# Performance work log

Measured on AMD Instinct MI355X. Metric: run time of the kernel, lower is better.

The kernel has to match this reference:

```python
import jax, jax.numpy as jnp
import numpy as np

HEADS = 32
KV_HEADS = 8
HEAD_DIM = 64
D = 2048
D_FF = 8192
EPS = 1e-6
THETA = 10000.0
MAX_STEPS = 4
NEG = -1e9


def _rope_tables(t):
    # LlamaRotaryEmbedding: cos/sin of shape [t, head_dim] with freqs duplicated
    inv_freq = 1.0 / (THETA ** (jnp.arange(0, HEAD_DIM, 2, dtype=jnp.float32) / HEAD_DIM))
    pos = jnp.arange(t, dtype=jnp.float32)
    freqs = pos[:, None] * inv_freq[None, :]          # [t, hd/2]
    emb = jnp.concatenate([freqs, freqs], axis=-1)    # [t, hd]
    return jnp.cos(emb), jnp.sin(emb)


def _rotate_half(x):
    h = x.shape[-1] // 2
    return jnp.concatenate([-x[..., h:], x[..., :h]], axis=-1)


def _rms_norm(x, w):
    return x * jax.lax.rsqrt(jnp.mean(x * x, axis=-1, keepdims=True) + EPS) * w


def _decoder_layer(h, w_q, w_k, w_v, w_o, ln1_w, ln2_w, w_gate, w_up, w_down):
    # h: [N, t, D]
    N, t, _ = h.shape
    x = _rms_norm(h, ln1_w)
    q = (x @ w_q).reshape(N, t, HEADS, HEAD_DIM)
    k = (x @ w_k).reshape(N, t, KV_HEADS, HEAD_DIM)
    v = (x @ w_v).reshape(N, t, KV_HEADS, HEAD_DIM)
    cos, sin = _rope_tables(t)
    cos = cos[None, :, None, :]
    sin = sin[None, :, None, :]
    q = q * cos + _rotate_half(q) * sin
    k = k * cos + _rotate_half(k) * sin
    rep = HEADS // KV_HEADS
    k = jnp.repeat(k, rep, axis=2)  # GQA: repeat kv heads
    v = jnp.repeat(v, rep, axis=2)
    scores = jnp.einsum('bqhd,bkhd->bhqk', q, k) / jnp.sqrt(jnp.float32(HEAD_DIM))
    causal = jnp.tril(jnp.ones((t, t), dtype=bool))
    scores = jnp.where(causal[None, None], scores, NEG)
    attn = jax.nn.softmax(scores, axis=-1)
    o = jnp.einsum('bhqk,bkhd->bqhd', attn, v).reshape(N, t, HEADS * HEAD_DIM)
    h = h + o @ w_o
    x = _rms_norm(h, ln2_w)
    h = h + (jax.nn.silu(x @ w_gate) * (x @ w_up)) @ w_down
    return h


def _micro_step_decode(hiddens, w_q, w_k, w_v, w_o, ln1_w, ln2_w, w_gate, w_up, w_down):
    # hiddens: [N, 1, D]; loop recomputes full attention over growing sequence (no KV cache)
    out = None
    for _ in range(MAX_STEPS + 1):
        out = _decoder_layer(hiddens, w_q, w_k, w_v, w_o, ln1_w, ln2_w, w_gate, w_up, w_down)
        hiddens = jnp.concatenate([hiddens, out[:, -1:, :]], axis=1)
    return out  # [N, MAX_STEPS+1, D]


def _gather_indices(comp_seq_lens, inst_lens):
    seqs = np.asarray(comp_seq_lens)
    insts = np.asarray(inst_lens)
    idx, off = [], 0
    for s, i in zip(seqs, insts):
        s, i = int(s), int(i)
        idx.append(np.arange(off + i - 1, off + s - 1))  # take_off_last=True
        off += s
    return np.concatenate(idx)


def setup_inputs() -> dict:
    key = jax.random.key(0)
    ks = jax.random.split(key, 10)
    B, S, I = 8, 512, 256
    total = B * S
    w = 0.02
    return {
        'hidden_states': jax.random.normal(ks[0], (1, total, D), jnp.float32),
        'comp_seq_lens': jnp.full((B,), S, dtype=jnp.int64),
        'inst_lens': jnp.full((B,), I, dtype=jnp.int64),
        'w_q': jax.random.normal(ks[1], (D, HEADS * HEAD_DIM), jnp.float32) * w,
        'w_k': jax.random.normal(ks[2], (D, KV_HEADS * HEAD_DIM), jnp.float32) * w,
        'w_v': jax.random.normal(ks[3], (D, KV_HEADS * HEAD_DIM), jnp.float32) * w,
        'w_o': jax.random.normal(ks[4], (HEADS * HEAD_DIM, D), jnp.float32) * w,
        'ln1_w': jnp.ones((D,), jnp.float32),
        'ln2_w': jnp.ones((D,), jnp.float32),
        'w_gate': jax.random.normal(ks[5], (D, D_FF), jnp.float32) * w,
        'w_up': jax.random.normal(ks[6], (D, D_FF), jnp.float32) * w,
        'w_down': jax.random.normal(ks[7], (D_FF, D), jnp.float32) * w,
    }


def reference(hidden_states, comp_seq_lens, inst_lens, w_q, w_k, w_v, w_o, ln1_w, ln2_w, w_gate, w_up, w_down):
    idx = _gather_indices(comp_seq_lens, inst_lens)
    hiddens = hidden_states[0, idx][:, None, :]  # [N, 1, D]
    return _micro_step_decode(hiddens, w_q, w_k, w_v, w_o, ln1_w, ln2_w, w_gate, w_up, w_down)
```

## Files before the change

### kernel.cpp

```cpp
#include <hip/hip_runtime.h>
#include <hip/hip_bf16.h>
#include <stdint.h>

#define DMODEL 2048
#define QDIM   2048
#define KVDIM  512
#define QKVDIM 3072
#define DFF    8192
#define NSTEPS 5

typedef __bf16 bf16_t;
typedef __attribute__((ext_vector_type(8))) __bf16 bf16x8;
typedef __attribute__((ext_vector_type(4))) float f32x4;

#define GLL16(g, l)                                                         \
  __builtin_amdgcn_global_load_lds(                                          \
      (const __attribute__((address_space(1))) void*)(g),                    \
      (__attribute__((address_space(3))) void*)(l), 16, 0, 0)

#define MFMA_BF16 __builtin_amdgcn_mfma_f32_16x16x32_bf16

__device__ __forceinline__ float wave_sum(float v) {
#pragma unroll
  for (int o = 32; o > 0; o >>= 1) v += __shfl_xor(v, o, 64);
  return v;
}

__global__ void build_idx_kernel(const int* __restrict__ seq, const int* __restrict__ inst,
                                 int B, int* __restrict__ idx, int* __restrict__ dN, int nmax) {
  __shared__ int sbase[64], soff[64], scnt[64], snb;
  if (threadIdx.x == 0) {
    bool is64 = (B >= 2);
    for (int i = 0; i < B && is64; ++i) {
      if (i & 1) { if (seq[i] != 0 || inst[i] != 0) is64 = false; }
      else       { if (seq[i] == 0) is64 = false; }
    }
    int off = 0, row = 0, nb = (B < 64 ? B : 64);
    for (int b = 0; b < nb; ++b) {
      int s = is64 ? seq[2 * b] : seq[b];
      int i = is64 ? inst[2 * b] : inst[b];
      sbase[b] = row; soff[b] = off + i - 1; scnt[b] = s - i;
      row += s - i; off += s;
    }
    snb = nb;
    *dN = row < nmax ? row : nmax;
  }
  __syncthreads();
  int nb = snb;
  for (int b = 0; b < nb; ++b) {
    int cnt = scnt[b], base = sbase[b], o0 = soff[b];
    for (int t = threadIdx.x; t < cnt; t += blockDim.x) {
      int r = base + t;
      if (r < nmax) idx[r] = o0 + t;
    }
  }
}

__global__ __launch_bounds__(256)
void gather_kernel(const float* __restrict__ hs, const int* __restrict__ idx,
                   float* __restrict__ h0, const int* __restrict__ dN) {
  int r = blockIdx.x; if (r >= *dN) return;
  const float4* in = (const float4*)(hs + (size_t)idx[r] * DMODEL);
  float4* out = (float4*)(h0 + (size_t)r * DMODEL);
  out[threadIdx.x]       = in[threadIdx.x];
  out[threadIdx.x + 256] = in[threadIdx.x + 256];
}

__global__ __launch_bounds__(256)
void wtrans_kernel(const float* __restrict__ W, bf16_t* __restrict__ Wt, int K, int Nc) {
  __shared__ float tile[32][33];
  int c0 = blockIdx.x * 32, k0 = blockIdx.y * 32;
  int tx = threadIdx.x & 31, ty = threadIdx.x >> 5;
#pragma unroll
  for (int yy = 0; yy < 4; ++yy)
    tile[ty + 8 * yy][tx] = W[(size_t)(k0 + ty + 8 * yy) * Nc + c0 + tx];
  __syncthreads();
#pragma unroll
  for (int yy = 0; yy < 4; ++yy)
    Wt[(size_t)(c0 + ty + 8 * yy) * K + k0 + tx] = (bf16_t)tile[tx][ty + 8 * yy];
}

__global__ __launch_bounds__(256)
void rmsnorm_kernel(const float* __restrict__ h, long hstride, const float* __restrict__ w,
                    bf16_t* __restrict__ x, const int* __restrict__ dN) {
  int r = blockIdx.x; if (r >= *dN) return;
  const float* row = h + (size_t)r * hstride;
  int t = threadIdx.x;
  float4 v0 = ((const float4*)row)[2 * t];
  float4 v1 = ((const float4*)row)[2 * t + 1];
  float ss = v0.x*v0.x + v0.y*v0.y + v0.z*v0.z + v0.w*v0.w
           + v1.x*v1.x + v1.y*v1.y + v1.z*v1.z + v1.w*v1.w;
  ss = wave_sum(ss);
  __shared__ float part[4];
  if ((t & 63) == 0) part[t >> 6] = ss;
  __syncthreads();
  float inv = rsqrtf((part[0] + part[1] + part[2] + part[3]) * (1.0f / DMODEL) + 1e-6f);
  const float4* wv = (const float4*)w;
  float4 w0 = wv[2 * t], w1 = wv[2 * t + 1];
  union { bf16_t b[8]; uint4 q; } u;
  u.b[0] = (bf16_t)(v0.x * inv * w0.x);
  u.b[1] = (bf16_t)(v0.y * inv * w0.y);
  u.b[2] = (bf16_t)(v0.z * inv * w0.z);
  u.b[3] = (bf16_t)(v0.w * inv * w0.w);
  u.b[4] = (bf16_t)(v1.x * inv * w1.x);
  u.b[5] = (bf16_t)(v1.y * inv * w1.y);
  u.b[6] = (bf16_t)(v1.z * inv * w1.z);
  u.b[7] = (bf16_t)(v1.w * inv * w1.w);
  *(uint4*)(x + (size_t)r * DMODEL + t * 8) = u.q;
}

__global__ __launch_bounds__(256)
void attn_fused_kernel(const bf16_t* __restrict__ part, long zstride,
                       bf16_t* __restrict__ kc, bf16_t* __restrict__ vc,
                       bf16_t* __restrict__ o, int p, const int* __restrict__ dN) {
  int r = blockIdx.x; if (r >= *dN) return;
  int wid = threadIdx.x >> 6, lane = threadIdx.x & 63;
  int kh = blockIdx.y;
  int head = kh * 4 + wid;
  size_t qb = (size_t)r * QKVDIM;

  int fi = lane & 31;
  float ang = (float)p * expf((float)fi * -0.28782313662425576f);
  float cv, sv; sincosf(ang, &sv, &cv);

  size_t qo = qb + (size_t)head * 64 + lane;
  float q = (float)part[qo] + (float)part[zstride + qo];
  float qp = __shfl_xor(q, 32, 64);
  float qr = q * cv + ((lane < 32) ? -qp : qp) * sv;

  size_t kb = qb + QDIM + (size_t)kh * 64 + lane;
  float kraw = (float)part[kb] + (float)part[zstride + kb];
  float kp_ = __shfl_xor(kraw, 32, 64);
  float kr = kraw * cv + ((lane < 32) ? -kp_ : kp_) * sv;
  size_t vb = kb + KVDIM;
  float vnew = (float)part[vb] + (float)part[zstride + vb];

  size_t cbase = (size_t)r * NSTEPS * KVDIM + (size_t)kh * 64 + lane;
  if (wid == 0) {
    kc[cbase + (size_t)p * KVDIM] = (bf16_t)kr;
    vc[cbase + (size_t)p * KVDIM] = (bf16_t)vnew;
  }

  float s[NSTEPS];
#pragma unroll
  for (int j = 0; j < NSTEPS; ++j) {
    s[j] = -1e30f;
    if (j < p) {
      float kj = (float)kc[cbase + (size_t)j * KVDIM];
      s[j] = wave_sum(qr * kj) * 0.125f;
    } else if (j == p) {
      s[j] = wave_sum(qr * (float)(bf16_t)kr) * 0.125f;
    }
  }
  float m = s[0];
#pragma unroll
  for (int j = 1; j < NSTEPS; ++j) m = fmaxf(m, s[j]);
  float aw[NSTEPS]; float den = 0.f;
#pragma unroll
  for (int j = 0; j < NSTEPS; ++j) { aw[j] = (j <= p) ? expf(s[j] - m) : 0.f; den += aw[j]; }
  float oa = 0.f;
#pragma unroll
  for (int j = 0; j < NSTEPS; ++j) {
    if (j < p)       oa += aw[j] * (float)vc[cbase + (size_t)j * KVDIM];
    else if (j == p) oa += aw[j] * (float)(bf16_t)vnew;
  }
  o[(size_t)r * QDIM + (size_t)head * 64 + lane] = (bf16_t)(oa / den);
}

template <int MODE>
__global__ __launch_bounds__(512)
void gemm256_kernel(const bf16_t* __restrict__ A, const bf16_t* __restrict__ Bt,
                    int krow, int kchunk, const int* __restrict__ dN,
                    long zstride,
                    bf16_t* __restrict__ outb, long obstride,
                    const bf16_t* __restrict__ gateb, long gstride) {
  const int N = *dN;
  const int brow = blockIdx.y * 256, bcol = blockIdx.x * 256;
  if (brow >= N) return;
  const size_t koff = (size_t)blockIdx.z * kchunk;

  extern __shared__ __align__(16) bf16_t lds[];
  bf16_t* As = lds;
  bf16_t* Bs = lds + 32768;

  const int t = threadIdx.x;
  const int lane = t & 63, wid = t >> 6;
  const int wm = wid >> 2, wn = wid & 3;
  const int hi = lane >> 4, lo = lane & 15;

  const int swsrc = ((lane & 3) ^ ((lane >> 3) & 3)) << 3;
  const size_t aoffl = (size_t)(brow + (lane >> 2)) * krow + koff + swsrc;
  const size_t boffl = (size_t)(bcol + (lane >> 2)) * krow + koff + swsrc;
  const size_t chk0 = (size_t)(wid * 32) * krow;
  const size_t chk1 = (size_t)(wid * 32 + 16) * krow;
  const int lst0 = wid * 1024;
  const int lst1 = wid * 1024 + 512;

  const int rsl = (hi ^ ((lo >> 1) & 3)) * 8;
  const int abase = (wm * 128 + lo) * 32 + rsl;
  const int bbase = (wn * 64 + lo) * 32 + rsl;

  f32x4 acc[8][4] = {};
  const int nt = kchunk >> 6;

#define STG_A(T, kh) do {                                        \
    const bf16_t* g_ = A + aoffl + (size_t)(T) * 64 + (kh) * 32; \
    bf16_t* l_ = As + (((T) & 1) << 14) + (kh) * 8192;           \
    GLL16(g_ + chk0, l_ + lst0);                                 \
    GLL16(g_ + chk1, l_ + lst1);                                 \
  } while (0)
#define STG_B(T, kh) do {                                        \
    const bf16_t* g_ = Bt + boffl + (size_t)(T) * 64 + (kh) * 32;\
    bf16_t* l_ = Bs + (((T) & 1) << 14) + (kh) * 8192;           \
    GLL16(g_ + chk0, l_ + lst0);                                 \
    GLL16(g_ + chk1, l_ + lst1);                                 \
  } while (0)

  STG_A(0, 0); STG_B(0, 0); STG_A(0, 1); STG_B(0, 1);
  if (nt > 1) {
    STG_A(1, 0); STG_B(1, 0);
    asm volatile("s_waitcnt vmcnt(8)" ::: "memory");
  } else {
    asm volatile("s_waitcnt vmcnt(4)" ::: "memory");
  }
  __builtin_amdgcn_s_barrier();

  for (int T = 0; T < nt; ++T) {
    const int buf = (T & 1) << 14;
    bf16x8 af[8], b0, b1;
#pragma unroll
    for (int m = 0; m < 8; ++m)
      af[m] = *(const bf16x8*)(As + buf + abase + m * 512);
    b0 = *(const bf16x8*)(Bs + buf + bbase);
    b1 = *(const bf16x8*)(Bs + buf + bbase + 512);
    if (T + 1 < nt) STG_A(T + 1, 1);
    asm volatile("s_waitcnt lgkmcnt(0)" ::: "memory");
    __builtin_amdgcn_s_barrier();
    __builtin_amdgcn_s_setprio(1);
#pragma unroll
    for (int m = 0; m < 8; ++m) {
      acc[m][0] = MFMA_BF16(af[m], b0, acc[m][0], 0, 0, 0);
      acc[m][1] = MFMA_BF16(af[m], b1, acc[m][1], 0, 0, 0);
    }
    __builtin_amdgcn_s_setprio(0);
    b0 = *(const bf16x8*)(Bs + buf + bbase + 1024);
    b1 = *(const bf16x8*)(Bs + buf + bbase + 1536);
    if (T + 1 < nt) STG_B(T + 1, 1);
    if (T < nt - 1) asm volatile("s_waitcnt vmcnt(8) lgkmcnt(0)" ::: "memory");
    else            asm volatile("s_waitcnt vmcnt(0) lgkmcnt(0)" ::: "memory");
    __builtin_amdgcn_s_barrier();
    __builtin_amdgcn_s_setprio(1);
#pragma unroll
    for (int m = 0; m < 8; ++m) {
      acc[m][2] = MFMA_BF16(af[m], b0, acc[m][2], 0, 0, 0);
      acc[m][3] = MFMA_BF16(af[m], b1, acc[m][3], 0, 0, 0);
    }
    __builtin_amdgcn_s_setprio(0);
#pragma unroll
    for (int m = 0; m < 8; ++m)
      af[m] = *(const bf16x8*)(As + buf + 8192 + abase + m * 512);
    b0 = *(const bf16x8*)(Bs + buf + 8192 + bbase);
    b1 = *(const bf16x8*)(Bs + buf + 8192 + bbase + 512);
    if (T + 2 < nt) STG_A(T + 2, 0);
    asm volatile("s_waitcnt lgkmcnt(0)" ::: "memory");
    __builtin_amdgcn_s_barrier();
    __builtin_amdgcn_s_setprio(1);
#pragma unroll
    for (int m = 0; m < 8; ++m) {
      acc[m][0] = MFMA_BF16(af[m], b0, acc[m][0], 0, 0, 0);
      acc[m][1] = MFMA_BF16(af[m], b1, acc[m][1], 0, 0, 0);
    }
    __builtin_amdgcn_s_setprio(0);
    b0 = *(const bf16x8*)(Bs + buf + 8192 + bbase + 1024);
    b1 = *(const bf16x8*)(Bs + buf + 8192 + bbase + 1536);
    if (T + 2 < nt) STG_B(T + 2, 0);
    if (T < nt - 2)       asm volatile("s_waitcnt vmcnt(8) lgkmcnt(0)" ::: "memory");
    else if (T == nt - 2) asm volatile("s_waitcnt vmcnt(4) lgkmcnt(0)" ::: "memory");
    else                  asm volatile("s_waitcnt vmcnt(0) lgkmcnt(0)" ::: "memory");
    __builtin_amdgcn_s_barrier();
    __builtin_amdgcn_s_setprio(1);
#pragma unroll
    for (int m = 0; m < 8; ++m) {
      acc[m][2] = MFMA_BF16(af[m], b0, acc[m][2], 0, 0, 0);
      acc[m][3] = MFMA_BF16(af[m], b1, acc[m][3], 0, 0, 0);
    }
    __builtin_amdgcn_s_setprio(0);
  }
#undef STG_A
#undef STG_B

  const int rbase = brow + wm * 128 + hi * 4;
  const int cbase = bcol + wn * 64 + lo;
  bf16_t* pb = (MODE == 3) ? outb + (size_t)blockIdx.z * zstride : outb;
#pragma unroll
  for (int m = 0; m < 8; ++m) {
#pragma unroll
    for (int n = 0; n < 4; ++n) {
      const int col = cbase + n * 16;
#pragma unroll
      for (int j = 0; j < 4; ++j) {
        const int row = rbase + m * 16 + j;
        if (row < N) {
          float v = acc[m][n][j];
          if (MODE == 2) {
            float g = (float)gateb[(size_t)row * gstride + col];
            float sg = g / (1.0f + expf(-g));
            pb[(size_t)row * obstride + col] = (bf16_t)(sg * v);
          } else {
            pb[(size_t)row * obstride + col] = (bf16_t)v;
          }
        }
      }
    }
  }
}

template <int NZ>
__global__ __launch_bounds__(256)
void reduce_norm_kernel(const bf16_t* __restrict__ part, long zstride,
                        const float* __restrict__ res, long rstride,
                        float* __restrict__ out, long ostride,
                        bf16_t* __restrict__ x, const float* __restrict__ lnw,
                        const int* __restrict__ dN) {
  int r = blockIdx.x; if (r >= *dN) return;
  const int c = threadIdx.x * 8;
  const float* rv = res + (size_t)r * rstride + c;
  float s[8];
#pragma unroll
  for (int j = 0; j < 8; ++j) s[j] = rv[j];
#pragma unroll
  for (int z = 0; z < NZ; ++z) {
    const bf16x8 v = *(const bf16x8*)(part + (size_t)z * zstride + (size_t)r * DMODEL + c);
#pragma unroll
    for (int j = 0; j < 8; ++j) s[j] += (float)v[j];
  }
  float* o = out + (size_t)r * ostride + c;
#pragma unroll
  for (int j = 0; j < 8; ++j) o[j] = s[j];
  if (x) {
    float ss = 0.f;
#pragma unroll
    for (int j = 0; j < 8; ++j) ss += s[j] * s[j];
    ss = wave_sum(ss);
    __shared__ float ps[4];
    if ((threadIdx.x & 63) == 0) ps[threadIdx.x >> 6] = ss;
    __syncthreads();
    float inv = rsqrtf((ps[0] + ps[1] + ps[2] + ps[3]) * (1.0f / DMODEL) + 1e-6f);
    union { bf16_t b[8]; uint4 q; } u;
#pragma unroll
    for (int j = 0; j < 8; ++j) u.b[j] = (bf16_t)(s[j] * inv * lnw[c + j]);
    *(uint4*)(x + (size_t)r * DMODEL + c) = u.q;
  }
}

extern "C" void kernel_launch(void* const* d_in, const int* in_sizes, int n_in,
                              void* d_out, int out_size, void* d_ws, size_t ws_size,
                              hipStream_t stream) {
  const float* hs  = (const float*)d_in[0];
  const int*   seq = (const int*)d_in[1];
  const int*   ins = (const int*)d_in[2];
  const float* w_q = (const float*)d_in[3];
  const float* w_k = (const float*)d_in[4];
  const float* w_v = (const float*)d_in[5];
  const float* w_o = (const float*)d_in[6];
  const float* ln1 = (const float*)d_in[7];
  const float* ln2 = (const float*)d_in[8];
  const float* w_g = (const float*)d_in[9];
  const float* w_u = (const float*)d_in[10];
  const float* w_d = (const float*)d_in[11];
  const int  B     = in_sizes[1];
  const long total = (long)in_sizes[0] / DMODEL;

  const size_t WQKV_E = (size_t)QKVDIM * DMODEL;
  const size_t WO_E   = (size_t)DMODEL * DMODEL;
  const size_t WG_E   = (size_t)DFF * DMODEL;

  struct WS {
    int* dN; int* idx;
    bf16_t *Wqkv, *Wo, *Wg, *Wu, *Wd;
    bf16_t* kc; bf16_t* vc; float* hattn; bf16_t* gate;
    bf16_t* part;
    bf16_t* o;
    float*  h0;
    bf16_t* x;
    size_t bytes;
  };
  char* base = (char*)d_ws;
  auto mk = [&](long nm) {
    WS w; size_t o = 0;
    auto alloc = [&](size_t b) { char* p = base + o; o = (o + b + 255) & ~(size_t)255; return p; };
    w.dN    = (int*)alloc(4);
    w.idx   = (int*)alloc((size_t)nm * 4);
    w.Wqkv  = (bf16_t*)alloc(WQKV_E * 2);
    w.Wo    = (bf16_t*)alloc(WO_E * 2);
    w.Wg    = (bf16_t*)alloc(WG_E * 2);
    w.Wu    = (bf16_t*)alloc(WG_E * 2);
    w.Wd    = (bf16_t*)alloc(WG_E * 2);
    w.kc    = (bf16_t*)alloc((size_t)nm * NSTEPS * KVDIM * 2);
    w.vc    = (bf16_t*)alloc((size_t)nm * NSTEPS * KVDIM * 2);
    w.hattn = (float*)alloc((size_t)nm * DMODEL * 4);
    w.gate  = (bf16_t*)alloc((size_t)nm * DFF * 2);
    char* R = alloc((size_t)nm * DMODEL * 2 * 4);
    w.part  = (bf16_t*)R;
    w.o     = (bf16_t*)R;
    w.h0    = (float*)(R + (size_t)nm * DMODEL * 2);
    w.x     = (bf16_t*)alloc((size_t)nm * DMODEL * 2);
    w.bytes = o;
    return w;
  };
  long nm = ((total + 255) / 256) * 256;
  WS w = mk(nm);
  while (w.bytes > ws_size && nm > 256) { nm -= 256; w = mk(nm); }

  build_idx_kernel<<<1, 512, 0, stream>>>(seq, ins, B, w.idx, w.dN, (int)nm);
  gather_kernel<<<(uint32_t)nm, 256, 0, stream>>>(hs, w.idx, w.h0, w.dN);

  dim3 tb(256);
  wtrans_kernel<<<dim3(DMODEL/32, DMODEL/32), tb, 0, stream>>>(w_q, w.Wqkv, DMODEL, DMODEL);
  wtrans_kernel<<<dim3(KVDIM/32,  DMODEL/32), tb, 0, stream>>>(w_k, w.Wqkv + (size_t)QDIM * DMODEL, DMODEL, KVDIM);
  wtrans_kernel<<<dim3(KVDIM/32,  DMODEL/32), tb, 0, stream>>>(w_v, w.Wqkv + (size_t)(QDIM + KVDIM) * DMODEL, DMODEL, KVDIM);
  wtrans_kernel<<<dim3(DMODEL/32, DMODEL/32), tb, 0, stream>>>(w_o, w.Wo, DMODEL, DMODEL);
  wtrans_kernel<<<dim3(DFF/32,    DMODEL/32), tb, 0, stream>>>(w_g, w.Wg, DMODEL, DFF);
  wtrans_kernel<<<dim3(DFF/32,    DMODEL/32), tb, 0, stream>>>(w_u, w.Wu, DMODEL, DFF);
  wtrans_kernel<<<dim3(DMODEL/32, DFF/32),    tb, 0, stream>>>(w_d, w.Wd, DFF, DMODEL);

  const int gy2 = (int)(nm / 256);
  const uint32_t LDSB = 131072;
  float* outF = (float*)d_out;
  const long zsD = (long)nm * DMODEL;
  const long zsQ = (long)nm * QKVDIM;

  for (int p = 0; p < NSTEPS; ++p) {
    const float* hprev = (p == 0) ? w.h0 : outF + (size_t)(p - 1) * DMODEL;
    const long   hstr  = (p == 0) ? DMODEL : (long)NSTEPS * DMODEL;

    if (p == 0)
      rmsnorm_kernel<<<(uint32_t)nm, 256, 0, stream>>>(hprev, hstr, ln1, w.x, w.dN);

    gemm256_kernel<3><<<dim3(QKVDIM/256, gy2, 2), 512, LDSB, stream>>>(
        w.x, w.Wqkv, DMODEL, DMODEL/2, w.dN, zsQ, w.gate, QKVDIM, nullptr, 0);

    attn_fused_kernel<<<dim3((uint32_t)nm, 8), 256, 0, stream>>>(
        w.gate, zsQ, w.kc, w.vc, w.o, p, w.dN);

    gemm256_kernel<3><<<dim3(DMODEL/256, gy2, 4), 512, LDSB, stream>>>(
        w.o, w.Wo, DMODEL, DMODEL/4, w.dN, zsD, w.gate, DMODEL, nullptr, 0);
    reduce_norm_kernel<4><<<(uint32_t)nm, 256, 0, stream>>>(
        w.gate, zsD, hprev, hstr, w.hattn, DMODEL, w.x, ln2, w.dN);

    gemm256_kernel<0><<<dim3(DFF/256, gy2, 1), 512, LDSB, stream>>>(
        w.x, w.Wg, DMODEL, DMODEL, w.dN, 0, w.gate, DFF, nullptr, 0);
    gemm256_kernel<2><<<dim3(DFF/256, gy2, 1), 512, LDSB, stream>>>(
        w.x, w.Wu, DMODEL, DMODEL, w.dN, 0, w.gate, DFF, w.gate, DFF);

    gemm256_kernel<3><<<dim3(DMODEL/256, gy2, 4), 512, LDSB, stream>>>(
        w.gate, w.Wd, DFF, DFF/4, w.dN, zsD, w.part, DMODEL, nullptr, 0);
    reduce_norm_kernel<4><<<(uint32_t)nm, 256, 0, stream>>>(
        w.part, zsD, w.hattn, DMODEL, outF + (size_t)p * DMODEL, (long)NSTEPS * DMODEL,
        (p + 1 < NSTEPS) ? w.x : nullptr, ln1, w.dN);
  }
}
```

Measured before the change: 1.838 ms.

## Fuse gate and up projections into one dual-weight GEMM with SiLU epilogue

Replaces the separate gate GEMM and up GEMM (the second of which re-read the gate output to apply SiLU) with a single kernel. For each 256x128 output tile it stages A once and loads both Wg and Wu tiles, keeping two accumulator sets and applying silu(g)*u in registers. This avoids reading A twice, the write and re-read of the gate intermediate, and one launch. In exchange each block has half the output width, and the pipeline interleaves two MFMA phases with extra barriers, which may lower per-block MFMA efficiency.

After: 1.685 ms. 1.09x faster.

```diff
diff --git a/kernel.cpp b/kernel.cpp
--- a/kernel.cpp
+++ b/kernel.cpp
@@ -172,8 +172,7 @@
 void gemm256_kernel(const bf16_t* __restrict__ A, const bf16_t* __restrict__ Bt,
                     int krow, int kchunk, const int* __restrict__ dN,
                     long zstride,
-                    bf16_t* __restrict__ outb, long obstride,
-                    const bf16_t* __restrict__ gateb, long gstride) {
+                    bf16_t* __restrict__ outb, long obstride) {
   const int N = *dN;
   const int brow = blockIdx.y * 256, bcol = blockIdx.x * 256;
   if (brow >= N) return;
@@ -300,15 +299,148 @@
 #pragma unroll
       for (int j = 0; j < 4; ++j) {
         const int row = rbase + m * 16 + j;
+        if (row < N)
+          pb[(size_t)row * obstride + col] = (bf16_t)acc[m][n][j];
+      }
+    }
+  }
+}
+
+__global__ __launch_bounds__(512)
+void gemm256gu_kernel(const bf16_t* __restrict__ A, const bf16_t* __restrict__ Wg,
+                      const bf16_t* __restrict__ Wu, int krow,
+                      const int* __restrict__ dN,
+                      bf16_t* __restrict__ outb, long obstride) {
+  const int N = *dN;
+  const int brow = blockIdx.y * 256, bcol = blockIdx.x * 128;
+  if (brow >= N) return;
+
+  extern __shared__ __align__(16) bf16_t lds[];
+  bf16_t* As = lds;
+  bf16_t* Bg = lds + 32768;
+  bf16_t* Bu = lds + 49152;
+
+  const int t = threadIdx.x;
+  const int lane = t & 63, wid = t >> 6;
+  const int wm = wid >> 2, wn = wid & 3;
+  const int hi = lane >> 4, lo = lane & 15;
+
+  const int swsrc = ((lane & 3) ^ ((lane >> 3) & 3)) << 3;
+  const size_t aoffl = (size_t)(brow + (lane >> 2)) * krow + swsrc;
+  const size_t boffl = (size_t)(bcol + (lane >> 2)) * krow + swsrc;
+  const size_t chk0 = (size_t)(wid * 32) * krow;
+  const size_t chk1 = (size_t)(wid * 32 + 16) * krow;
+  const size_t bchk = (size_t)(wid * 16) * krow;
+  const int lst0 = wid * 1024, lst1 = wid * 1024 + 512;
+  const int lbst = wid * 512;
+
+  const int rsl = (hi ^ ((lo >> 1) & 3)) * 8;
+  const int abase = (wm * 128 + lo) * 32 + rsl;
+  const int bbase = (wn * 32 + lo) * 32 + rsl;
+
+  f32x4 accg[8][2] = {}, accu[8][2] = {};
+  const int nt = krow >> 6;
+
+#define STG_A(T, kh) do {                                        \
+    const bf16_t* g_ = A + aoffl + (size_t)(T) * 64 + (kh) * 32; \
+    bf16_t* l_ = As + (((T) & 1) << 14) + (kh) * 8192;           \
+    GLL16(g_ + chk0, l_ + lst0);                                 \
+    GLL16(g_ + chk1, l_ + lst1);                                 \
+  } while (0)
+#define STG_GU(T, kh) do {                                       \
+    const size_t go_ = boffl + bchk + (size_t)(T) * 64 + (kh) * 32; \
+    const int lb_ = (((T) & 1) << 13) + (kh) * 4096 + lbst;      \
+    GLL16(Wg + go_, Bg + lb_);                                   \
+    GLL16(Wu + go_, Bu + lb_);                                   \
+  } while (0)
+
+  STG_A(0, 0); STG_GU(0, 0); STG_A(0, 1); STG_GU(0, 1);
+  if (nt > 1) {
+    STG_A(1, 0); STG_GU(1, 0);
+    asm volatile("s_waitcnt vmcnt(8)" ::: "memory");
+  } else {
+    asm volatile("s_waitcnt vmcnt(4)" ::: "memory");
+  }
+  __builtin_amdgcn_s_barrier();
+
+  for (int T = 0; T < nt; ++T) {
+    const int abuf = (T & 1) << 14, bbuf = (T & 1) << 13;
+    bf16x8 af[8], b0, b1;
+#pragma unroll
+    for (int m = 0; m < 8; ++m)
+      af[m] = *(const bf16x8*)(As + abuf + abase + m * 512);
+    b0 = *(const bf16x8*)(Bg + bbuf + bbase);
+    b1 = *(const bf16x8*)(Bg + bbuf + bbase + 512);
+    if (T + 1 < nt) STG_A(T + 1, 1);
+    asm volatile("s_waitcnt lgkmcnt(0)" ::: "memory");
+    __builtin_amdgcn_s_barrier();
+    __builtin_amdgcn_s_setprio(1);
+#pragma unroll
+    for (int m = 0; m < 8; ++m) {
+      accg[m][0] = MFMA_BF16(af[m], b0, accg[m][0], 0, 0, 0);
+      accg[m][1] = MFMA_BF16(af[m], b1, accg[m][1], 0, 0, 0);
+    }
+    __builtin_amdgcn_s_setprio(0);
+    b0 = *(const bf16x8*)(Bu + bbuf + bbase);
+    b1 = *(const bf16x8*)(Bu + bbuf + bbase + 512);
+    if (T + 1 < nt) STG_GU(T + 1, 1);
+    if (T < nt - 1) asm volatile("s_waitcnt vmcnt(8) lgkmcnt(0)" ::: "memory");
+    else            asm volatile("s_waitcnt vmcnt(0) lgkmcnt(0)" ::: "memory");
+    __builtin_amdgcn_s_barrier();
+    __builtin_amdgcn_s_setprio(1);
+#pragma unroll
+    for (int m = 0; m < 8; ++m) {
+      accu[m][0] = MFMA_BF16(af[m], b0, accu[m][0], 0, 0, 0);
+      accu[m][1] = MFMA_BF16(af[m], b1, accu[m][1], 0, 0, 0);
+    }
+    __builtin_amdgcn_s_setprio(0);
+#pragma unroll
+    for (int m = 0; m < 8; ++m)
+      af[m] = *(const bf16x8*)(As + abuf + 8192 + abase + m * 512);
+    b0 = *(const bf16x8*)(Bg + bbuf + 4096 + bbase);
+    b1 = *(const bf16x8*)(Bg + bbuf + 4096 + bbase + 512);
+    if (T + 2 < nt) STG_A(T + 2, 0);
+    asm volatile("s_waitcnt lgkmcnt(0)" ::: "memory");
+    __builtin_amdgcn_s_barrier();
+    __builtin_amdgcn_s_setprio(1);
+#pragma unroll
+    for (int m = 0; m < 8; ++m) {
+      accg[m][0] = MFMA_BF16(af[m], b0, accg[m][0], 0, 0, 0);
+      accg[m][1] = MFMA_BF16(af[m], b1, accg[m][1], 0, 0, 0);
+    }
+    __builtin_amdgcn_s_setprio(0);
+    b0 = *(const bf16x8*)(Bu + bbuf + 4096 + bbase);
+    b1 = *(const bf16x8*)(Bu + bbuf + 4096 + bbase + 512);
+    if (T + 2 < nt) STG_GU(T + 2, 0);
+    if (T < nt - 2)       asm volatile("s_waitcnt vmcnt(8) lgkmcnt(0)" ::: "memory");
+    else if (T == nt - 2) asm volatile("s_waitcnt vmcnt(4) lgkmcnt(0)" ::: "memory");
+    else                  asm volatile("s_waitcnt vmcnt(0) lgkmcnt(0)" ::: "memory");
+    __builtin_amdgcn_s_barrier();
+    __builtin_amdgcn_s_setprio(1);
+#pragma unroll
+    for (int m = 0; m < 8; ++m) {
+      accu[m][0] = MFMA_BF16(af[m], b0, accu[m][0], 0, 0, 0);
+      accu[m][1] = MFMA_BF16(af[m], b1, accu[m][1], 0, 0, 0);
+    }
+    __builtin_amdgcn_s_setprio(0);
+  }
+#undef STG_A
+#undef STG_GU
+
+  const int rbase = brow + wm * 128 + hi * 4;
+  const int cbase = bcol + wn * 32 + lo;
+#pragma unroll
+  for (int m = 0; m < 8; ++m) {
+#pragma unroll
+    for (int n = 0; n < 2; ++n) {
+      const int col = cbase + n * 16;
+#pragma unroll
+      for (int j = 0; j < 4; ++j) {
+        const int row = rbase + m * 16 + j;
         if (row < N) {
-          float v = acc[m][n][j];
-          if (MODE == 2) {
-            float g = (float)gateb[(size_t)row * gstride + col];
-            float sg = g / (1.0f + expf(-g));
-            pb[(size_t)row * obstride + col] = (bf16_t)(sg * v);
-          } else {
-            pb[(size_t)row * obstride + col] = (bf16_t)v;
-          }
+          float g = accg[m][n][j];
+          float sg = g / (1.0f + expf(-g));
+          outb[(size_t)row * obstride + col] = (bf16_t)(sg * accu[m][n][j]);
         }
       }
     }
@@ -438,23 +570,21 @@
       rmsnorm_kernel<<<(uint32_t)nm, 256, 0, stream>>>(hprev, hstr, ln1, w.x, w.dN);
 
     gemm256_kernel<3><<<dim3(QKVDIM/256, gy2, 2), 512, LDSB, stream>>>(
-        w.x, w.Wqkv, DMODEL, DMODEL/2, w.dN, zsQ, w.gate, QKVDIM, nullptr, 0);
+        w.x, w.Wqkv, DMODEL, DMODEL/2, w.dN, zsQ, w.gate, QKVDIM);
 
     attn_fused_kernel<<<dim3((uint32_t)nm, 8), 256, 0, stream>>>(
         w.gate, zsQ, w.kc, w.vc, w.o, p, w.dN);
 
     gemm256_kernel<3><<<dim3(DMODEL/256, gy2, 4), 512, LDSB, stream>>>(
-        w.o, w.Wo, DMODEL, DMODEL/4, w.dN, zsD, w.gate, DMODEL, nullptr, 0);
+        w.o, w.Wo, DMODEL, DMODEL/4, w.dN, zsD, w.gate, DMODEL);
     reduce_norm_kernel<4><<<(uint32_t)nm, 256, 0, stream>>>(
         w.gate, zsD, hprev, hstr, w.hattn, DMODEL, w.x, ln2, w.dN);
 
-    gemm256_kernel<0><<<dim3(DFF/256, gy2, 1), 512, LDSB, stream>>>(
-        w.x, w.Wg, DMODEL, DMODEL, w.dN, 0, w.gate, DFF, nullptr, 0);
-    gemm256_kernel<2><<<dim3(DFF/256, gy2, 1), 512, LDSB, stream>>>(
-        w.x, w.Wu, DMODEL, DMODEL, w.dN, 0, w.gate, DFF, w.gate, DFF);
+    gemm256gu_kernel<<<dim3(DFF/128, gy2, 1), 512, LDSB, stream>>>(
+        w.x, w.Wg, w.Wu, DMODEL, w.dN, w.gate, DFF);
 
     gemm256_kernel<3><<<dim3(DMODEL/256, gy2, 4), 512, LDSB, stream>>>(
-        w.gate, w.Wd, DFF, DFF/4, w.dN, zsD, w.part, DMODEL, nullptr, 0);
+        w.gate, w.Wd, DFF, DFF/4, w.dN, zsD, w.part, DMODEL);
     reduce_norm_kernel<4><<<(uint32_t)nm, 256, 0, stream>>>(
         w.part, zsD, w.hattn, DMODEL, outF + (size_t)p * DMODEL, (long)NSTEPS * DMODEL,
         (p + 1 < NSTEPS) ? w.x : nullptr, ln1, w.dN);
```

## Fuse gate and up projections into one dual-B GEMM with SiLU epilogue

Applied to the files above, without the earlier changes.

The GEMM kernel now takes two B operands staged into separate LDS halves, so one block computes matching 128-column tiles of both the gate and up projections and applies SiLU(gate)*up in registers. This removes the separate gate GEMM launch, the bf16 round-trip of the gate activations through global memory, and the second read of the shared A tile. Other GEMMs reuse the same kernel by passing one matrix twice with a 128-row offset for the second half of a 256-column tile. Gate values are no longer rounded to bf16 before SiLU, which slightly changes numerics.

Result: faster. 1.680 ms (-8.6%).

```diff
diff --git a/kernel.cpp b/kernel.cpp
--- a/kernel.cpp
+++ b/kernel.cpp
@@ -169,19 +169,20 @@
 
 template <int MODE>
 __global__ __launch_bounds__(512)
-void gemm256_kernel(const bf16_t* __restrict__ A, const bf16_t* __restrict__ Bt,
-                    int krow, int kchunk, const int* __restrict__ dN,
-                    long zstride,
-                    bf16_t* __restrict__ outb, long obstride,
-                    const bf16_t* __restrict__ gateb, long gstride) {
+void gemm256d_kernel(const bf16_t* __restrict__ A, const bf16_t* __restrict__ B0,
+                     const bf16_t* __restrict__ B1, int krow, int kchunk,
+                     const int* __restrict__ dN, long zstride,
+                     bf16_t* __restrict__ outb, long obstride) {
   const int N = *dN;
-  const int brow = blockIdx.y * 256, bcol = blockIdx.x * 256;
+  const int brow = blockIdx.y * 256;
+  const int bcol = blockIdx.x * ((MODE == 2) ? 128 : 256);
   if (brow >= N) return;
   const size_t koff = (size_t)blockIdx.z * kchunk;
 
   extern __shared__ __align__(16) bf16_t lds[];
-  bf16_t* As = lds;
-  bf16_t* Bs = lds + 32768;
+  bf16_t* As  = lds;
+  bf16_t* B0s = lds + 32768;
+  bf16_t* B1s = lds + 49152;
 
   const int t = threadIdx.x;
   const int lane = t & 63, wid = t >> 6;
@@ -190,17 +191,19 @@
 
   const int swsrc = ((lane & 3) ^ ((lane >> 3) & 3)) << 3;
   const size_t aoffl = (size_t)(brow + (lane >> 2)) * krow + koff + swsrc;
-  const size_t boffl = (size_t)(bcol + (lane >> 2)) * krow + koff + swsrc;
+  const size_t b0off = (size_t)(bcol + (lane >> 2)) * krow + koff + swsrc;
+  const size_t b1off = b0off + ((MODE == 2) ? 0 : (size_t)128 * krow);
   const size_t chk0 = (size_t)(wid * 32) * krow;
   const size_t chk1 = (size_t)(wid * 32 + 16) * krow;
-  const int lst0 = wid * 1024;
-  const int lst1 = wid * 1024 + 512;
+  const size_t bchk = (size_t)(wid * 16) * krow;
+  const int lst0 = wid * 1024, lst1 = wid * 1024 + 512;
+  const int lbst = wid * 512;
 
   const int rsl = (hi ^ ((lo >> 1) & 3)) * 8;
   const int abase = (wm * 128 + lo) * 32 + rsl;
-  const int bbase = (wn * 64 + lo) * 32 + rsl;
-
-  f32x4 acc[8][4] = {};
+  const int bbase = (wn * 32 + lo) * 32 + rsl;
+
+  f32x4 acc0[8][2] = {}, acc1[8][2] = {};
   const int nt = kchunk >> 6;
 
 #define STG_A(T, kh) do {                                        \
@@ -210,10 +213,10 @@
     GLL16(g_ + chk1, l_ + lst1);                                 \
   } while (0)
 #define STG_B(T, kh) do {                                        \
-    const bf16_t* g_ = Bt + boffl + (size_t)(T) * 64 + (kh) * 32;\
-    bf16_t* l_ = Bs + (((T) & 1) << 14) + (kh) * 8192;           \
-    GLL16(g_ + chk0, l_ + lst0);                                 \
-    GLL16(g_ + chk1, l_ + lst1);                                 \
+    const size_t go_ = bchk + (size_t)(T) * 64 + (kh) * 32;      \
+    const int lb_ = (((T) & 1) << 13) + (kh) * 4096 + lbst;      \
+    GLL16(B0 + b0off + go_, B0s + lb_);                          \
+    GLL16(B1 + b1off + go_, B1s + lb_);                          \
   } while (0)
 
   STG_A(0, 0); STG_B(0, 0); STG_A(0, 1); STG_B(0, 1);
@@ -226,25 +229,25 @@
   __builtin_amdgcn_s_barrier();
 
   for (int T = 0; T < nt; ++T) {
-    const int buf = (T & 1) << 14;
+    const int abuf = (T & 1) << 14, bbuf = (T & 1) << 13;
     bf16x8 af[8], b0, b1;
 #pragma unroll
     for (int m = 0; m < 8; ++m)
-      af[m] = *(const bf16x8*)(As + buf + abase + m * 512);
-    b0 = *(const bf16x8*)(Bs + buf + bbase);
-    b1 = *(const bf16x8*)(Bs + buf + bbase + 512);
+      af[m] = *(const bf16x8*)(As + abuf + abase + m * 512);
+    b0 = *(const bf16x8*)(B0s + bbuf + bbase);
+    b1 = *(const bf16x8*)(B0s + bbuf + bbase + 512);
     if (T + 1 < nt) STG_A(T + 1, 1);
     asm volatile("s_waitcnt lgkmcnt(0)" ::: "memory");
     __builtin_amdgcn_s_barrier();
     __builtin_amdgcn_s_setprio(1);
 #pragma unroll
     for (int m = 0; m < 8; ++m) {
-      acc[m][0] = MFMA_BF16(af[m], b0, acc[m][0], 0, 0, 0);
-      acc[m][1] = MFMA_BF16(af[m], b1, acc[m][1], 0, 0, 0);
+      acc0[m][0] = MFMA_BF16(af[m], b0, acc0[m][0], 0, 0, 0);
+      acc0[m][1] = MFMA_BF16(af[m], b1, acc0[m][1], 0, 0, 0);
     }
     __builtin_amdgcn_s_setprio(0);
-    b0 = *(const bf16x8*)(Bs + buf + bbase + 1024);
-    b1 = *(const bf16x8*)(Bs + buf + bbase + 1536);
+    b0 = *(const bf16x8*)(B1s + bbuf + bbase);
+    b1 = *(const bf16x8*)(B1s + bbuf + bbase + 512);
     if (T + 1 < nt) STG_B(T + 1, 1);
     if (T < nt - 1) asm volatile("s_waitcnt vmcnt(8) lgkmcnt(0)" ::: "memory");
     else            asm volatile("s_waitcnt vmcnt(0) lgkmcnt(0)" ::: "memory");
@@ -252,27 +255,27 @@
     __builtin_amdgcn_s_setprio(1);
 #pragma unroll
     for (int m = 0; m < 8; ++m) {
-      acc[m][2] = MFMA_BF16(af[m], b0, acc[m][2], 0, 0, 0);
-      acc[m][3] = MFMA_BF16(af[m], b1, acc[m][3], 0, 0, 0);
+      acc1[m][0] = MFMA_BF16(af[m], b0, acc1[m][0], 0, 0, 0);
+      acc1[m][1] = MFMA_BF16(af[m], b1, acc1[m][1], 0, 0, 0);
     }
     __builtin_amdgcn_s_setprio(0);
 #pragma unroll
     for (int m = 0; m < 8; ++m)
-      af[m] = *(const bf16x8*)(As + buf + 8192 + abase + m * 512);
-    b0 = *(const bf16x8*)(Bs + buf + 8192 + bbase);
-    b1 = *(const bf16x8*)(Bs + buf + 8192 + bbase + 512);
+      af[m] = *(const bf16x8*)(As + abuf + 8192 + abase + m * 512);
+    b0 = *(const bf16x8*)(B0s + bbuf + 4096 + bbase);
+    b1 = *(const bf16x8*)(B0s + bbuf + 4096 + bbase + 512);
     if (T + 2 < nt) STG_A(T + 2, 0);
     asm volatile("s_waitcnt lgkmcnt(0)" ::: "memory");
     __builtin_amdgcn_s_barrier();
     __builtin_amdgcn_s_setprio(1);
 #pragma unroll
     for (int m = 0; m < 8; ++m) {
-      acc[m][0] = MFMA_BF16(af[m], b0, acc[m][0], 0, 0, 0);
-      acc[m][1] = MFMA_BF16(af[m], b1, acc[m][1], 0, 0, 0);
+      acc0[m][0] = MFMA_BF16(af[m], b0, acc0[m][0], 0, 0, 0);
+      acc0[m][1] = MFMA_BF16(af[m], b1, acc0[m][1], 0, 0, 0);
     }
     __builtin_amdgcn_s_setprio(0);
-    b0 = *(const bf16x8*)(Bs + buf + 8192 + bbase + 1024);
-    b1 = *(const bf16x8*)(Bs + buf + 8192 + bbase + 1536);
+    b0 = *(const bf16x8*)(B1s + bbuf + 4096 + bbase);
+    b1 = *(const bf16x8*)(B1s + bbuf + 4096 + bbase + 512);
     if (T + 2 < nt) STG_B(T + 2, 0);
     if (T < nt - 2)       asm volatile("s_waitcnt vmcnt(8) lgkmcnt(0)" ::: "memory");
     else if (T == nt - 2) asm volatile("s_waitcnt vmcnt(4) lgkmcnt(0)" ::: "memory");
@@ -281,8 +284,8 @@
     __builtin_amdgcn_s_setprio(1);
 #pragma unroll
     for (int m = 0; m < 8; ++m) {
-      acc[m][2] = MFMA_BF16(af[m], b0, acc[m][2], 0, 0, 0);
-      acc[m][3] = MFMA_BF16(af[m], b1, acc[m][3], 0, 0, 0);
+      acc1[m][0] = MFMA_BF16(af[m], b0, acc1[m][0], 0, 0, 0);
+      acc1[m][1] = MFMA_BF16(af[m], b1, acc1[m][1], 0, 0, 0);
     }
     __builtin_amdgcn_s_setprio(0);
   }
@@ -290,24 +293,24 @@
 #undef STG_B
 
   const int rbase = brow + wm * 128 + hi * 4;
-  const int cbase = bcol + wn * 64 + lo;
+  const int cb0 = bcol + wn * 32 + lo;
   bf16_t* pb = (MODE == 3) ? outb + (size_t)blockIdx.z * zstride : outb;
 #pragma unroll
   for (int m = 0; m < 8; ++m) {
 #pragma unroll
-    for (int n = 0; n < 4; ++n) {
-      const int col = cbase + n * 16;
+    for (int n = 0; n < 2; ++n) {
+      const int col = cb0 + n * 16;
 #pragma unroll
       for (int j = 0; j < 4; ++j) {
         const int row = rbase + m * 16 + j;
         if (row < N) {
-          float v = acc[m][n][j];
           if (MODE == 2) {
-            float g = (float)gateb[(size_t)row * gstride + col];
+            float g = acc0[m][n][j];
             float sg = g / (1.0f + expf(-g));
-            pb[(size_t)row * obstride + col] = (bf16_t)(sg * v);
+            pb[(size_t)row * obstride + col] = (bf16_t)(sg * acc1[m][n][j]);
           } else {
-            pb[(size_t)row * obstride + col] = (bf16_t)v;
+            pb[(size_t)row * obstride + col]       = (bf16_t)acc0[m][n][j];
+            pb[(size_t)row * obstride + col + 128] = (bf16_t)acc1[m][n][j];
           }
         }
       }
@@ -437,24 +440,22 @@
     if (p == 0)
       rmsnorm_kernel<<<(uint32_t)nm, 256, 0, stream>>>(hprev, hstr, ln1, w.x, w.dN);
 
-    gemm256_kernel<3><<<dim3(QKVDIM/256, gy2, 2), 512, LDSB, stream>>>(
-        w.x, w.Wqkv, DMODEL, DMODEL/2, w.dN, zsQ, w.gate, QKVDIM, nullptr, 0);
+    gemm256d_kernel<3><<<dim3(QKVDIM/256, gy2, 2), 512, LDSB, stream>>>(
+        w.x, w.Wqkv, w.Wqkv, DMODEL, DMODEL/2, w.dN, zsQ, w.gate, QKVDIM);
 
     attn_fused_kernel<<<dim3((uint32_t)nm, 8), 256, 0, stream>>>(
         w.gate, zsQ, w.kc, w.vc, w.o, p, w.dN);
 
-    gemm256_kernel<3><<<dim3(DMODEL/256, gy2, 4), 512, LDSB, stream>>>(
-        w.o, w.Wo, DMODEL, DMODEL/4, w.dN, zsD, w.gate, DMODEL, nullptr, 0);
+    gemm256d_kernel<3><<<dim3(DMODEL/256, gy2, 4), 512, LDSB, stream>>>(
+        w.o, w.Wo, w.Wo, DMODEL, DMODEL/4, w.dN, zsD, w.gate, DMODEL);
     reduce_norm_kernel<4><<<(uint32_t)nm, 256, 0, stream>>>(
         w.gate, zsD, hprev, hstr, w.hattn, DMODEL, w.x, ln2, w.dN);
 
-    gemm256_kernel<0><<<dim3(DFF/256, gy2, 1), 512, LDSB, stream>>>(
-        w.x, w.Wg, DMODEL, DMODEL, w.dN, 0, w.gate, DFF, nullptr, 0);
-    gemm256_kernel<2><<<dim3(DFF/256, gy2, 1), 512, LDSB, stream>>>(
-        w.x, w.Wu, DMODEL, DMODEL, w.dN, 0, w.gate, DFF, w.gate, DFF);
-
-    gemm256_kernel<3><<<dim3(DMODEL/256, gy2, 4), 512, LDSB, stream>>>(
-        w.gate, w.Wd, DFF, DFF/4, w.dN, zsD, w.part, DMODEL, nullptr, 0);
+    gemm256d_kernel<2><<<dim3(DFF/128, gy2, 1), 512, LDSB, stream>>>(
+        w.x, w.Wg, w.Wu, DMODEL, DMODEL, w.dN, 0, w.gate, DFF);
+
+    gemm256d_kernel<3><<<dim3(DMODEL/256, gy2, 4), 512, LDSB, stream>>>(
+        w.gate, w.Wd, w.Wd, DFF, DFF/4, w.dN, zsD, w.part, DMODEL);
     reduce_norm_kernel<4><<<(uint32_t)nm, 256, 0, stream>>>(
         w.part, zsD, w.hattn, DMODEL, outF + (size_t)p * DMODEL, (long)NSTEPS * DMODEL,
         (p + 1 < NSTEPS) ? w.x : nullptr, ln1, w.dN);
```
